# Performance work log

Measured on AMD Instinct MI355X. Metric: run time of the kernel, lower is better.

Reference implementation:

```python
import math
import jax, jax.numpy as jnp
import numpy as np

E = 24  # num experts


def layer_norm(x, w, b, eps=1e-6):
    m = x.mean(-1, keepdims=True)
    v = x.var(-1, keepdims=True)
    return (x - m) / jnp.sqrt(v + eps) * w + b


def top2_dispatch(x, Wg, C):
    # x: [S, d] -> combine/dispatch: [S, E, C] (GShard/DeepSpeed top-2 gating)
    logits = x @ Wg                                   # [S, E]
    gates = jax.nn.softmax(logits, axis=-1)
    idx1 = jnp.argmax(gates, axis=-1)
    m1 = jax.nn.one_hot(idx1, E, dtype=x.dtype)       # [S, E]
    masked = jnp.where(m1 > 0, -jnp.inf, logits)
    idx2 = jnp.argmax(masked, axis=-1)
    m2 = jax.nn.one_hot(idx2, E, dtype=x.dtype)
    # position of each token within its expert's capacity buffer
    loc1 = jnp.cumsum(m1, axis=0) - m1
    loc2 = jnp.cumsum(m2, axis=0) - m2 + jnp.sum(m1, axis=0, keepdims=True)
    m1 = m1 * (loc1 < C)                              # drop overflow tokens
    m2 = m2 * (loc2 < C)
    g1 = jnp.sum(gates * m1, axis=-1)
    g2 = jnp.sum(gates * m2, axis=-1)
    denom = jnp.maximum(g1 + g2, 1e-9)
    g1, g2 = g1 / denom, g2 / denom
    p1 = jnp.sum(loc1 * m1, axis=-1).astype(jnp.int32)
    p2 = jnp.sum(loc2 * m2, axis=-1).astype(jnp.int32)
    c1 = g1[:, None, None] * m1[:, :, None] * jax.nn.one_hot(p1, C, dtype=x.dtype)[:, None, :]
    c2 = g2[:, None, None] * m2[:, :, None] * jax.nn.one_hot(p2, C, dtype=x.dtype)[:, None, :]
    combine = c1 + c2                                  # [S, E, C]
    dispatch = (combine > 0).astype(x.dtype)
    return combine, dispatch


def moe_apply(x, combine, dispatch, W, b):
    # dispatch tokens to expert buffers, per-expert GEMM, combine back
    disp = jnp.einsum('sec,sd->ecd', dispatch, x)      # [E, C, d]
    h = jnp.einsum('ecd,edf->ecf', disp, W) + b[:, None, :]
    return jnp.einsum('sec,ecf->sf', combine, h)       # [S, f]


def setup_inputs() -> dict:
    b, seq, d_in, d_hid = 4, 2048, 1024, 4096
    ks = jax.random.split(jax.random.key(0), 6)
    s = 0.02
    return {
        'x': jax.random.normal(ks[0], (b, seq, d_in), dtype=jnp.float32),
        'Wg': jax.random.normal(ks[1], (d_in, E), dtype=jnp.float32) * s,
        'W1': jax.random.normal(ks[2], (E, d_in, d_hid), dtype=jnp.float32) * s,
        'b1': jnp.zeros((E, d_hid), dtype=jnp.float32),
        'W2': jax.random.normal(ks[3], (E, d_hid, d_in), dtype=jnp.float32) * s,
        'b2': jnp.zeros((E, d_in), dtype=jnp.float32),
        'ln_hid_w': jnp.ones((4, d_hid), dtype=jnp.float32),
        'ln_hid_b': jnp.zeros((4, d_hid), dtype=jnp.float32),
        'ln_out_w': jnp.ones((d_in,), dtype=jnp.float32),
        'ln_out_b': jnp.zeros((d_in,), dtype=jnp.float32),
    }


def reference(x, Wg, W1, b1, W2, b2, ln_hid_w, ln_hid_b, ln_out_w, ln_out_b):
    bsz, seq, d = x.shape
    H = 4
    n = seq // H
    S = bsz * n  # tokens per sub-sequence MoE call
    C = math.ceil(2 * S / E)  # top-2 capacity, capacity_factor=1.0
    # b (h n) c -> h (b n) c
    xg = x.reshape(bsz, H, n, d).transpose(1, 0, 2, 3).reshape(H, S, d)

    def per_group(xf, lw, lb):
        combine, dispatch = top2_dispatch(xf, Wg, C)
        h = moe_apply(xf, combine, dispatch, W1, b1)       # [S, d_hid]
        h = layer_norm(h, lw, lb)
        h = jax.nn.relu(h)                                  # dropout = identity (eval)
        return moe_apply(h, combine, dispatch, W2, b2)      # reuse gate_decision

    out = jax.vmap(per_group)(xg, ln_hid_w, ln_hid_b)       # [H, S, d]
    out = out.reshape(H, bsz, n, d).transpose(1, 0, 2, 3).reshape(bsz, seq, d)
    return layer_norm(out + x, ln_out_w, ln_out_b)
```

## Files before the change

### kernel.cpp

```cpp
#include <hip/hip_runtime.h>
#include <cstdint>
#include <cstddef>

#define E_      24
#define D_IN    1024
#define D_HID   4096
#define HGRP    4
#define BSZ     4
#define SEQ     2048
#define NSUB    512
#define S_      2048
#define NTOKG   8192
#define CAP     171
#define MR      768
#define MTILE   3
#define KSPL2   4

typedef __attribute__((ext_vector_type(4))) float          f32x4;
typedef __attribute__((ext_vector_type(4))) unsigned short u16x4;
typedef __attribute__((ext_vector_type(8))) unsigned short u16x8;
typedef __attribute__((ext_vector_type(4))) unsigned int   u32x4;
typedef __attribute__((ext_vector_type(8))) short          s16x8;

__device__ __forceinline__ unsigned short f2bf(float f) {
  unsigned int u = __float_as_uint(f);
  u += 0x7fffu + ((u >> 16) & 1u);
  return (unsigned short)(u >> 16);
}
__device__ __forceinline__ float bf2f(unsigned short v) {
  return __uint_as_float(((unsigned int)v) << 16);
}

__global__ __launch_bounds__(64)
void k_gating(const float* __restrict__ x, const float* __restrict__ Wg,
              int* __restrict__ tokE1, int* __restrict__ tokE2,
              float* __restrict__ tokG1, float* __restrict__ tokG2) {
  int tg = blockIdx.x;
  int h = tg >> 11, s = tg & 2047;
  int bi = s >> 9, ni = s & 511;
  const float* xr = x + ((size_t)bi*SEQ + (size_t)h*NSUB + ni) * D_IN;
  int lane = threadIdx.x;
  float acc[E_];
  #pragma unroll
  for (int e = 0; e < E_; ++e) acc[e] = 0.f;
  #pragma unroll
  for (int it = 0; it < D_IN/256; ++it) {
    f32x4 xv = *(const f32x4*)(xr + it*256 + lane*4);
    #pragma unroll
    for (int j = 0; j < 4; ++j) {
      float xs = xv[j];
      const float* wrow = Wg + (size_t)(it*256 + lane*4 + j) * E_;
      #pragma unroll
      for (int e = 0; e < E_; ++e) acc[e] += xs * wrow[e];
    }
  }
  #pragma unroll
  for (int e = 0; e < E_; ++e) {
    float v = acc[e];
    v += __shfl_xor(v, 32); v += __shfl_xor(v, 16); v += __shfl_xor(v, 8);
    v += __shfl_xor(v, 4);  v += __shfl_xor(v, 2);  v += __shfl_xor(v, 1);
    acc[e] = v;
  }
  if (lane == 0) {
    float mx = acc[0];
    #pragma unroll
    for (int e = 1; e < E_; ++e) mx = fmaxf(mx, acc[e]);
    float den = 0.f;
    #pragma unroll
    for (int e = 0; e < E_; ++e) den += expf(acc[e] - mx);
    int i1 = 0; float v1 = acc[0];
    #pragma unroll
    for (int e = 1; e < E_; ++e) if (acc[e] > v1) { v1 = acc[e]; i1 = e; }
    int i2 = -1; float v2 = -3.4e38f;
    #pragma unroll
    for (int e = 0; e < E_; ++e) if (e != i1 && acc[e] > v2) { v2 = acc[e]; i2 = e; }
    tokE1[tg] = i1; tokE2[tg] = i2;
    tokG1[tg] = expf(v1 - mx) / den;
    tokG2[tg] = expf(v2 - mx) / den;
  }
}

__global__ void k_init_slots(int* __restrict__ slotTok) {
  slotTok[blockIdx.x*256 + threadIdx.x] = -1;
}

__global__ __launch_bounds__(64)
void k_scan(const int* __restrict__ tokE1, const int* __restrict__ tokE2,
            float* __restrict__ tokG1, float* __restrict__ tokG2,
            int* __restrict__ tokP1, int* __restrict__ tokP2,
            int* __restrict__ slotTok) {
  int h = blockIdx.x;
  int lane = threadIdx.x;
  __shared__ int cnt[64][E_];
  __shared__ int tot1[E_];
  const int CH = S_/64;
  const int* e1 = tokE1 + h*S_;
  const int* e2 = tokE2 + h*S_;
  #pragma unroll
  for (int e = 0; e < E_; ++e) cnt[lane][e] = 0;
  __syncthreads();
  for (int k = 0; k < CH; ++k) cnt[lane][e1[lane*CH + k]]++;
  __syncthreads();
  if (lane < E_) {
    int run = 0;
    for (int j = 0; j < 64; ++j) { int t = cnt[j][lane]; cnt[j][lane] = run; run += t; }
    tot1[lane] = run;
  }
  __syncthreads();
  for (int k = 0; k < CH; ++k) {
    int s = lane*CH + k;
    int e = e1[s];
    int p = cnt[lane][e]++;
    int tg = h*S_ + s;
    if (p < CAP) { tokP1[tg] = p; slotTok[e*MR + h*CAP + p] = tg; }
    else         { tokP1[tg] = -1; }
  }
  __syncthreads();
  #pragma unroll
  for (int e = 0; e < E_; ++e) cnt[lane][e] = 0;
  __syncthreads();
  for (int k = 0; k < CH; ++k) cnt[lane][e2[lane*CH + k]]++;
  __syncthreads();
  if (lane < E_) {
    int run = tot1[lane];
    for (int j = 0; j < 64; ++j) { int t = cnt[j][lane]; cnt[j][lane] = run; run += t; }
  }
  __syncthreads();
  for (int k = 0; k < CH; ++k) {
    int s = lane*CH + k;
    int e = e2[s];
    int p = cnt[lane][e]++;
    int tg = h*S_ + s;
    if (p < CAP) { tokP2[tg] = p; slotTok[e*MR + h*CAP + p] = tg; }
    else         { tokP2[tg] = -1; }
  }
  __syncthreads();
  for (int k = 0; k < CH; ++k) {
    int tg = h*S_ + k*64 + lane;
    float g1 = (tokP1[tg] >= 0) ? tokG1[tg] : 0.f;
    float g2 = (tokP2[tg] >= 0) ? tokG2[tg] : 0.f;
    float den = fmaxf(g1 + g2, 1e-9f);
    tokG1[tg] = g1 / den;
    tokG2[tg] = g2 / den;
  }
}

__global__ __launch_bounds__(256)
void k_gather1(const float* __restrict__ x, const int* __restrict__ slotTok,
               unsigned short* __restrict__ A1) {
  int row = blockIdx.x;
  int tok = slotTok[row];
  int t = threadIdx.x;
  int k = t*4;
  int ba = ((k & 63)*2) ^ ((row & 7) << 4);
  char* dst = (char*)A1 + (size_t)row*(D_IN*2) + (size_t)(k >> 6)*128 + ba;
  u16x4 pk;
  if (tok >= 0) {
    int h = tok >> 11, s = tok & 2047;
    int bi = s >> 9, ni = s & 511;
    const float* xr = x + ((size_t)bi*SEQ + (size_t)h*NSUB + ni) * D_IN;
    f32x4 v = *(const f32x4*)(xr + k);
    pk.x = f2bf(v.x); pk.y = f2bf(v.y); pk.z = f2bf(v.z); pk.w = f2bf(v.w);
  } else {
    pk.x = 0; pk.y = 0; pk.z = 0; pk.w = 0;
  }
  *(u16x4*)dst = pk;
}

template<int K, int N>
__global__ __launch_bounds__(256)
void k_cvtW(const float* __restrict__ W, unsigned short* __restrict__ Wt) {
  const int NB = N/64, KB = K/64;
  int bid = blockIdx.x;
  int kb = bid % KB;
  int rem = bid / KB;
  int nb = rem % NB;
  int e  = rem / NB;
  __shared__ float lds[64][65];
  int t = threadIdx.x;
  int kl = t >> 2, ng = (t & 3) * 16;
  const float* src = W + ((size_t)e*K + (size_t)kb*64 + kl)*N + (size_t)nb*64 + ng;
  f32x4 v0 = *(const f32x4*)(src);
  f32x4 v1 = *(const f32x4*)(src + 4);
  f32x4 v2 = *(const f32x4*)(src + 8);
  f32x4 v3 = *(const f32x4*)(src + 12);
  #pragma unroll
  for (int j = 0; j < 4; ++j) lds[ng +  0 + j][kl] = v0[j];
  #pragma unroll
  for (int j = 0; j < 4; ++j) lds[ng +  4 + j][kl] = v1[j];
  #pragma unroll
  for (int j = 0; j < 4; ++j) lds[ng +  8 + j][kl] = v2[j];
  #pragma unroll
  for (int j = 0; j < 4; ++j) lds[ng + 12 + j][kl] = v3[j];
  __syncthreads();
  int nl = t >> 2, kg = (t & 3) * 16;
  u16x8 c0, c1;
  #pragma unroll
  for (int j = 0; j < 8; ++j) {
    c0[j] = f2bf(lds[nl][kg + j]);
    c1[j] = f2bf(lds[nl][kg + 8 + j]);
  }
  char* dst = (char*)Wt + ((size_t)e*N + (size_t)nb*64 + nl)*(K*2) + (size_t)kb*128;
  int sw = (nl & 7) << 4;
  *(u16x8*)(dst + ((kg*2)      ^ sw)) = c0;
  *(u16x8*)(dst + ((kg*2 + 16) ^ sw)) = c1;
}

template<int KROW, int KCHUNK, int N>
__global__ __launch_bounds__(512, 2)
void k_gemm(const unsigned short* __restrict__ A, const unsigned short* __restrict__ Wt,
            const float* __restrict__ bias, unsigned short* __restrict__ Out) {
  const int NT = N / 256;
  const int KSPLIT = KROW / KCHUNK;
  const int NKT = KCHUNK / 64;
  int cpx = gridDim.x >> 3;
  int lb = blockIdx.x;
  int bid = (lb & 7) * cpx + (lb >> 3);
  int mt  = bid % MTILE;
  int rem = bid / MTILE;
  int kc  = rem % KSPLIT;
  rem /= KSPLIT;
  int nt  = rem % NT;
  int e   = rem / NT;

  const char* Ab = (const char*)A  + ((size_t)e*MR + (size_t)mt*256) * (KROW*2);
  const char* Bb = (const char*)Wt + ((size_t)e*N  + (size_t)nt*256) * (KROW*2);
  size_t kbase = (size_t)kc * (KCHUNK*2);

  __shared__ unsigned short As0[256*64];
  __shared__ unsigned short As1[256*64];
  __shared__ unsigned short Bs0[256*64];
  __shared__ unsigned short Bs1[256*64];

  int tid  = threadIdx.x;
  int lane = tid & 63;
  int wid  = tid >> 6;
  int wr = wid >> 2, wc = wid & 3;

  f32x4 acc[8][4];
  #pragma unroll
  for (int i = 0; i < 8; ++i)
    #pragma unroll
    for (int j = 0; j < 4; ++j) acc[i][j] = (f32x4)0.f;

  auto stage = [&](int kt2, unsigned short* As, unsigned short* Bs) {
    size_t koff = kbase + (size_t)kt2*128;
    #pragma unroll
    for (int i = 0; i < 4; ++i) {
      int L = i*8192 + tid*16;
      __builtin_amdgcn_global_load_lds(
          (const __attribute__((address_space(1))) void*)(Ab + (size_t)(L >> 7)*(KROW*2) + koff + (L & 127)),
          (__attribute__((address_space(3))) void*)((char*)As + L), 16, 0, 0);
    }
    #pragma unroll
    for (int i = 0; i < 4; ++i) {
      int L = i*8192 + tid*16;
      __builtin_amdgcn_global_load_lds(
          (const __attribute__((address_space(1))) void*)(Bb + (size_t)(L >> 7)*(KROW*2) + koff + (L & 127)),
          (__attribute__((address_space(3))) void*)((char*)Bs + L), 16, 0, 0);
    }
  };
  auto fragsA = [&](const unsigned short* As, int ra, int ks, s16x8* afr) {
    int kb = ks*64 + (lane >> 4)*16;
    #pragma unroll
    for (int i = 0; i < 4; ++i) {
      int r = wr*128 + ra*64 + i*16 + (lane & 15);
      afr[i] = *(const s16x8*)((const char*)As + r*128 + (kb ^ ((r & 7) << 4)));
    }
  };
  auto fragsB = [&](const unsigned short* Bs, int ks, s16x8* bfr) {
    int kb = ks*64 + (lane >> 4)*16;
    #pragma unroll
    for (int j = 0; j < 4; ++j) {
      int c = wc*64 + j*16 + (lane & 15);
      bfr[j] = *(const s16x8*)((const char*)Bs + c*128 + (kb ^ ((c & 7) << 4)));
    }
  };
  auto mfma16 = [&](int ra, const s16x8* afr, const s16x8* bfr) {
    __builtin_amdgcn_s_setprio(1);
    #pragma unroll
    for (int i = 0; i < 4; ++i)
      #pragma unroll
      for (int j = 0; j < 4; ++j)
        acc[ra*4+i][j] = __builtin_amdgcn_mfma_f32_16x16x32_bf16(afr[i], bfr[j], acc[ra*4+i][j], 0, 0, 0);
    __builtin_amdgcn_s_setprio(0);
  };

  auto tile = [&](int t, const unsigned short* Ac, const unsigned short* Bc,
                  unsigned short* An, unsigned short* Bn) {
    int tn = (t + 1 < NKT) ? t + 1 : t;
    s16x8 afr[4], bfr[4];
    stage(tn, An, Bn);
    fragsA(Ac, 0, 0, afr); fragsB(Bc, 0, bfr);
    __builtin_amdgcn_s_barrier();
    asm volatile("s_waitcnt lgkmcnt(0)" ::: "memory");
    __builtin_amdgcn_sched_barrier(0);
    mfma16(0, afr, bfr);
    __builtin_amdgcn_s_barrier();
    fragsA(Ac, 1, 0, afr);
    __builtin_amdgcn_s_barrier();
    asm volatile("s_waitcnt lgkmcnt(0)" ::: "memory");
    __builtin_amdgcn_sched_barrier(0);
    mfma16(1, afr, bfr);
    __builtin_amdgcn_s_barrier();
    fragsA(Ac, 0, 1, afr); fragsB(Bc, 1, bfr);
    __builtin_amdgcn_s_barrier();
    asm volatile("s_waitcnt lgkmcnt(0)" ::: "memory");
    __builtin_amdgcn_sched_barrier(0);
    mfma16(0, afr, bfr);
    __builtin_amdgcn_s_barrier();
    fragsA(Ac, 1, 1, afr);
    __builtin_amdgcn_s_barrier();
    asm volatile("s_waitcnt lgkmcnt(0)" ::: "memory");
    __builtin_amdgcn_sched_barrier(0);
    mfma16(1, afr, bfr);
    __syncthreads();
  };

  stage(0, As0, Bs0);
  __syncthreads();
  for (int kt = 0; kt < NKT; kt += 2) {
    tile(kt,     As0, Bs0, As1, Bs1);
    tile(kt + 1, As1, Bs1, As0, Bs0);
  }

  unsigned short* Op = Out + (size_t)kc * ((size_t)E_*MR*N);
  #pragma unroll
  for (int j = 0; j < 4; ++j) {
    int col = nt*256 + wc*64 + j*16 + (lane & 15);
    float bv = (kc == 0) ? bias[(size_t)e*N + col] : 0.f;
    #pragma unroll
    for (int i = 0; i < 8; ++i) {
      int rowb = mt*256 + wr*128 + i*16 + (lane >> 4)*4;
      #pragma unroll
      for (int r = 0; r < 4; ++r) {
        float v = acc[i][j][r] + bv;
        Op[(size_t)e*MR*N + (size_t)(rowb + r)*N + col] = f2bf(v);
      }
    }
  }
}

__global__ __launch_bounds__(256)
void k_zero_empty(const int* __restrict__ slotTok, unsigned short* __restrict__ A2) {
  int row = blockIdx.x;
  if (slotTok[row] >= 0) return;
  u32x4 z = (u32x4)0u;
  char* base = (char*)A2 + (size_t)row*(D_HID*2) + threadIdx.x*32;
  *(u32x4*)base = z;
  *(u32x4*)(base + 16) = z;
}

__global__ __launch_bounds__(256)
void k_combine_ln(const unsigned short* __restrict__ H1,
                  const int* __restrict__ tokE1, const int* __restrict__ tokE2,
                  const int* __restrict__ tokP1, const int* __restrict__ tokP2,
                  const float* __restrict__ tokG1, const float* __restrict__ tokG2,
                  const float* __restrict__ lnw, const float* __restrict__ lnb,
                  unsigned short* __restrict__ A2) {
  int tg = blockIdx.x;
  int h = tg >> 11;
  int p1 = tokP1[tg], p2 = tokP2[tg];
  if (p1 < 0 && p2 < 0) return;
  float g1 = tokG1[tg], g2 = tokG2[tg];
  long r1 = (p1 >= 0) ? ((long)tokE1[tg]*MR + h*CAP + p1) : -1;
  long r2 = (p2 >= 0) ? ((long)tokE2[tg]*MR + h*CAP + p2) : -1;
  int t = threadIdx.x;
  float v[16];
  float sum = 0.f, sq = 0.f;
  #pragma unroll
  for (int u = 0; u < 4; ++u) {
    int f = u*1024 + t*4;
    float a0 = 0.f, a1 = 0.f, a2 = 0.f, a3 = 0.f;
    if (r1 >= 0) {
      u16x4 q = *(const u16x4*)(H1 + (size_t)r1*D_HID + f);
      a0 += g1*bf2f(q.x); a1 += g1*bf2f(q.y); a2 += g1*bf2f(q.z); a3 += g1*bf2f(q.w);
    }
    if (r2 >= 0) {
      u16x4 q = *(const u16x4*)(H1 + (size_t)r2*D_HID + f);
      a0 += g2*bf2f(q.x); a1 += g2*bf2f(q.y); a2 += g2*bf2f(q.z); a3 += g2*bf2f(q.w);
    }
    v[u*4+0] = a0; v[u*4+1] = a1; v[u*4+2] = a2; v[u*4+3] = a3;
    sum += a0 + a1 + a2 + a3;
    sq  += a0*a0 + a1*a1 + a2*a2 + a3*a3;
  }
  #pragma unroll
  for (int o = 32; o; o >>= 1) { sum += __shfl_xor(sum, o); sq += __shfl_xor(sq, o); }
  __shared__ float redA[4], redB[4];
  int wid = t >> 6;
  if ((t & 63) == 0) { redA[wid] = sum; redB[wid] = sq; }
  __syncthreads();
  float S = redA[0] + redA[1] + redA[2] + redA[3];
  float Q = redB[0] + redB[1] + redB[2] + redB[3];
  float m = S * (1.f / D_HID);
  float var = Q * (1.f / D_HID) - m*m;
  float rs = rsqrtf(var + 1e-6f);
  #pragma unroll
  for (int u = 0; u < 4; ++u) {
    int f = u*1024 + t*4;
    u16x4 pk;
    float y0 = fmaxf((v[u*4+0]-m)*rs*lnw[h*D_HID+f+0] + lnb[h*D_HID+f+0], 0.f);
    float y1 = fmaxf((v[u*4+1]-m)*rs*lnw[h*D_HID+f+1] + lnb[h*D_HID+f+1], 0.f);
    float y2 = fmaxf((v[u*4+2]-m)*rs*lnw[h*D_HID+f+2] + lnb[h*D_HID+f+2], 0.f);
    float y3 = fmaxf((v[u*4+3]-m)*rs*lnw[h*D_HID+f+3] + lnb[h*D_HID+f+3], 0.f);
    pk.x = f2bf(y0); pk.y = f2bf(y1); pk.z = f2bf(y2); pk.w = f2bf(y3);
    int chunk = f >> 6;
    int ob = (f & 63)*2;
    if (r1 >= 0)
      *(u16x4*)((char*)A2 + (size_t)r1*(D_HID*2) + (size_t)chunk*128 + (ob ^ (((int)r1 & 7) << 4))) = pk;
    if (r2 >= 0)
      *(u16x4*)((char*)A2 + (size_t)r2*(D_HID*2) + (size_t)chunk*128 + (ob ^ (((int)r2 & 7) << 4))) = pk;
  }
}

__global__ __launch_bounds__(256)
void k_final(const unsigned short* __restrict__ H2p, const float* __restrict__ x,
             const int* __restrict__ tokE1, const int* __restrict__ tokE2,
             const int* __restrict__ tokP1, const int* __restrict__ tokP2,
             const float* __restrict__ tokG1, const float* __restrict__ tokG2,
             const float* __restrict__ lnw, const float* __restrict__ lnb,
             float* __restrict__ out) {
  const size_t PSTR = (size_t)E_*MR*D_IN;
  int tg = blockIdx.x;
  int h = tg >> 11, s = tg & 2047;
  int bi = s >> 9, ni = s & 511;
  size_t xoff = ((size_t)bi*SEQ + (size_t)h*NSUB + ni) * D_IN;
  int p1 = tokP1[tg], p2 = tokP2[tg];
  float g1 = tokG1[tg], g2 = tokG2[tg];
  int t = threadIdx.x;
  int f = t*4;
  f32x4 xv = *(const f32x4*)(x + xoff + f);
  float v0 = xv.x, v1 = xv.y, v2 = xv.z, v3 = xv.w;
  if (p1 >= 0) {
    size_t r1 = (size_t)tokE1[tg]*MR + h*CAP + p1;
    float a0 = 0.f, a1 = 0.f, a2 = 0.f, a3 = 0.f;
    #pragma unroll
    for (int p = 0; p < KSPL2; ++p) {
      u16x4 q = *(const u16x4*)(H2p + p*PSTR + r1*D_IN + f);
      a0 += bf2f(q.x); a1 += bf2f(q.y); a2 += bf2f(q.z); a3 += bf2f(q.w);
    }
    v0 += g1*a0; v1 += g1*a1; v2 += g1*a2; v3 += g1*a3;
  }
  if (p2 >= 0) {
    size_t r2 = (size_t)tokE2[tg]*MR + h*CAP + p2;
    float a0 = 0.f, a1 = 0.f, a2 = 0.f, a3 = 0.f;
    #pragma unroll
    for (int p = 0; p < KSPL2; ++p) {
      u16x4 q = *(const u16x4*)(H2p + p*PSTR + r2*D_IN + f);
      a0 += bf2f(q.x); a1 += bf2f(q.y); a2 += bf2f(q.z); a3 += bf2f(q.w);
    }
    v0 += g2*a0; v1 += g2*a1; v2 += g2*a2; v3 += g2*a3;
  }
  float sum = v0+v1+v2+v3, sq = v0*v0+v1*v1+v2*v2+v3*v3;
  #pragma unroll
  for (int o = 32; o; o >>= 1) { sum += __shfl_xor(sum, o); sq += __shfl_xor(sq, o); }
  __shared__ float redA[4], redB[4];
  int wid = t >> 6;
  if ((t & 63) == 0) { redA[wid] = sum; redB[wid] = sq; }
  __syncthreads();
  float S = redA[0] + redA[1] + redA[2] + redA[3];
  float Q = redB[0] + redB[1] + redB[2] + redB[3];
  float m = S * (1.f / D_IN);
  float var = Q * (1.f / D_IN) - m*m;
  float rs = rsqrtf(var + 1e-6f);
  f32x4 res;
  res.x = (v0 - m)*rs*lnw[f+0] + lnb[f+0];
  res.y = (v1 - m)*rs*lnw[f+1] + lnb[f+1];
  res.z = (v2 - m)*rs*lnw[f+2] + lnb[f+2];
  res.w = (v3 - m)*rs*lnw[f+3] + lnb[f+3];
  *(f32x4*)(out + xoff + f) = res;
}

extern "C" void kernel_launch(void* const* d_in, const int* in_sizes, int n_in,
                              void* d_out, int out_size, void* d_ws, size_t ws_size,
                              hipStream_t stream) {
  const float* x    = (const float*)d_in[0];
  const float* Wg   = (const float*)d_in[1];
  const float* W1   = (const float*)d_in[2];
  const float* b1   = (const float*)d_in[3];
  const float* W2   = (const float*)d_in[4];
  const float* b2   = (const float*)d_in[5];
  const float* lnhw = (const float*)d_in[6];
  const float* lnhb = (const float*)d_in[7];
  const float* lnow = (const float*)d_in[8];
  const float* lnob = (const float*)d_in[9];
  float* out = (float*)d_out;
  (void)in_sizes; (void)n_in; (void)out_size; (void)ws_size;

  char* ws = (char*)d_ws;
  size_t off = 0;
  auto take = [&](size_t bytes) -> char* {
    char* p = ws + off;
    off += (bytes + 255) & ~(size_t)255;
    return p;
  };
  int*   tokE1 = (int*)take(NTOKG*sizeof(int));
  int*   tokE2 = (int*)take(NTOKG*sizeof(int));
  int*   tokP1 = (int*)take(NTOKG*sizeof(int));
  int*   tokP2 = (int*)take(NTOKG*sizeof(int));
  float* tokG1 = (float*)take(NTOKG*sizeof(float));
  float* tokG2 = (float*)take(NTOKG*sizeof(float));
  int*   slotTok = (int*)take((size_t)E_*MR*sizeof(int));
  unsigned short* A1 = (unsigned short*)take((size_t)E_*MR*D_IN*2);
  unsigned short* H1 = (unsigned short*)take((size_t)E_*MR*D_HID*2);
  unsigned short* A2 = (unsigned short*)take((size_t)E_*MR*D_HID*2);
  unsigned short* Wt = (unsigned short*)take((size_t)E_*D_IN*D_HID*2);
  unsigned short* H2p = H1;

  k_init_slots<<<dim3(E_*MR/256), dim3(256), 0, stream>>>(slotTok);
  k_gating<<<dim3(NTOKG), dim3(64), 0, stream>>>(x, Wg, tokE1, tokE2, tokG1, tokG2);
  k_scan<<<dim3(HGRP), dim3(64), 0, stream>>>(tokE1, tokE2, tokG1, tokG2, tokP1, tokP2, slotTok);
  k_gather1<<<dim3(E_*MR), dim3(256), 0, stream>>>(x, slotTok, A1);
  k_cvtW<D_IN, D_HID><<<dim3(E_*(D_HID/64)*(D_IN/64)), dim3(256), 0, stream>>>(W1, Wt);
  k_gemm<D_IN, D_IN, D_HID><<<dim3(E_*(D_HID/256)*MTILE), dim3(512), 0, stream>>>(A1, Wt, b1, H1);
  k_zero_empty<<<dim3(E_*MR), dim3(256), 0, stream>>>(slotTok, A2);
  k_combine_ln<<<dim3(NTOKG), dim3(256), 0, stream>>>(H1, tokE1, tokE2, tokP1, tokP2,
                                                      tokG1, tokG2, lnhw, lnhb, A2);
  k_cvtW<D_HID, D_IN><<<dim3(E_*(D_IN/64)*(D_HID/64)), dim3(256), 0, stream>>>(W2, Wt);
  k_gemm<D_HID, D_IN, D_IN><<<dim3(E_*(D_IN/256)*MTILE*KSPL2), dim3(512), 0, stream>>>(A2, Wt, b2, H2p);
  k_final<<<dim3(NTOKG), dim3(256), 0, stream>>>(H2p, x, tokE1, tokE2, tokP1, tokP2,
                                                 tokG1, tokG2, lnow, lnob, out);
}
```

Baseline: 898.1 us.

## Interleave GEMM global-to-LDS staging with MFMA phases and use partial vmcnt waits

The GEMM main loop no longer issues all eight global-to-LDS loads for the next tile at once and ends each tile with a full __syncthreads. The loads are split into per-slice calls spread across the four MFMA phases, with `s_waitcnt vmcnt(2)` plus barriers so only the slices needed next must be resident. This lets A rows 64-127 and 192-255 stay in flight across the tile boundary. Separately, the weight-conversion kernel now reads rows with 16 threads per row in float4 chunks, giving more contiguous global loads. The risk is subtle ordering bugs, because vmcnt counts only the issuing wave's own loads and the scheme relies on the slice-to-row mapping.

```diff
diff --git a/kernel.cpp b/kernel.cpp
--- a/kernel.cpp
+++ b/kernel.cpp
@@ -178,20 +178,15 @@
   int e  = rem / NB;
   __shared__ float lds[64][65];
   int t = threadIdx.x;
-  int kl = t >> 2, ng = (t & 3) * 16;
-  const float* src = W + ((size_t)e*K + (size_t)kb*64 + kl)*N + (size_t)nb*64 + ng;
-  f32x4 v0 = *(const f32x4*)(src);
-  f32x4 v1 = *(const f32x4*)(src + 4);
-  f32x4 v2 = *(const f32x4*)(src + 8);
-  f32x4 v3 = *(const f32x4*)(src + 12);
-  #pragma unroll
-  for (int j = 0; j < 4; ++j) lds[ng +  0 + j][kl] = v0[j];
-  #pragma unroll
-  for (int j = 0; j < 4; ++j) lds[ng +  4 + j][kl] = v1[j];
-  #pragma unroll
-  for (int j = 0; j < 4; ++j) lds[ng +  8 + j][kl] = v2[j];
-  #pragma unroll
-  for (int j = 0; j < 4; ++j) lds[ng + 12 + j][kl] = v3[j];
+  int rl = t >> 4;
+  int cl = (t & 15) * 4;
+  const float* base = W + ((size_t)e*K + (size_t)kb*64)*N + (size_t)nb*64;
+  #pragma unroll
+  for (int p = 0; p < 4; ++p) {
+    int r = p*16 + rl;
+    f32x4 v = *(const f32x4*)(base + (size_t)r*N + cl);
+    lds[cl+0][r] = v.x; lds[cl+1][r] = v.y; lds[cl+2][r] = v.z; lds[cl+3][r] = v.w;
+  }
   __syncthreads();
   int nl = t >> 2, kg = (t & 3) * 16;
   u16x8 c0, c1;
@@ -243,22 +238,19 @@
     #pragma unroll
     for (int j = 0; j < 4; ++j) acc[i][j] = (f32x4)0.f;
 
-  auto stage = [&](int kt2, unsigned short* As, unsigned short* Bs) {
+  auto stageAi = [&](int kt2, unsigned short* As, int i) {
     size_t koff = kbase + (size_t)kt2*128;
-    #pragma unroll
-    for (int i = 0; i < 4; ++i) {
-      int L = i*8192 + tid*16;
-      __builtin_amdgcn_global_load_lds(
-          (const __attribute__((address_space(1))) void*)(Ab + (size_t)(L >> 7)*(KROW*2) + koff + (L & 127)),
-          (__attribute__((address_space(3))) void*)((char*)As + L), 16, 0, 0);
-    }
-    #pragma unroll
-    for (int i = 0; i < 4; ++i) {
-      int L = i*8192 + tid*16;
-      __builtin_amdgcn_global_load_lds(
-          (const __attribute__((address_space(1))) void*)(Bb + (size_t)(L >> 7)*(KROW*2) + koff + (L & 127)),
-          (__attribute__((address_space(3))) void*)((char*)Bs + L), 16, 0, 0);
-    }
+    int L = i*8192 + tid*16;
+    __builtin_amdgcn_global_load_lds(
+        (const __attribute__((address_space(1))) void*)(Ab + (size_t)(L >> 7)*(KROW*2) + koff + (L & 127)),
+        (__attribute__((address_space(3))) void*)((char*)As + L), 16, 0, 0);
+  };
+  auto stageBi = [&](int kt2, unsigned short* Bs, int i) {
+    size_t koff = kbase + (size_t)kt2*128;
+    int L = i*8192 + tid*16;
+    __builtin_amdgcn_global_load_lds(
+        (const __attribute__((address_space(1))) void*)(Bb + (size_t)(L >> 7)*(KROW*2) + koff + (L & 127)),
+        (__attribute__((address_space(3))) void*)((char*)Bs + L), 16, 0, 0);
   };
   auto fragsA = [&](const unsigned short* As, int ra, int ks, s16x8* afr) {
     int kb = ks*64 + (lane >> 4)*16;
@@ -286,42 +278,52 @@
     __builtin_amdgcn_s_setprio(0);
   };
 
-  auto tile = [&](int t, const unsigned short* Ac, const unsigned short* Bc,
-                  unsigned short* An, unsigned short* Bn) {
-    int tn = (t + 1 < NKT) ? t + 1 : t;
+  unsigned short *Acur = As0, *Anxt = As1, *Bcur = Bs0, *Bnxt = Bs1;
+
+  stageBi(0, Bcur, 0); stageBi(0, Bcur, 1); stageBi(0, Bcur, 2); stageBi(0, Bcur, 3);
+  stageAi(0, Acur, 0); stageAi(0, Acur, 2);
+  stageAi(0, Acur, 1); stageAi(0, Acur, 3);
+  asm volatile("s_waitcnt vmcnt(2)" ::: "memory");
+  __builtin_amdgcn_sched_barrier(0);
+  __builtin_amdgcn_s_barrier();
+
+  for (int kt = 0; kt < NKT; ++kt) {
+    int tn = (kt + 1 < NKT) ? kt + 1 : kt;
     s16x8 afr[4], bfr[4];
-    stage(tn, An, Bn);
-    fragsA(Ac, 0, 0, afr); fragsB(Bc, 0, bfr);
+    fragsA(Acur, 0, 0, afr); fragsB(Bcur, 0, bfr);
+    stageBi(tn, Bnxt, 0); stageBi(tn, Bnxt, 1);
+    asm volatile("s_waitcnt vmcnt(2)" ::: "memory");
+    __builtin_amdgcn_sched_barrier(0);
     __builtin_amdgcn_s_barrier();
     asm volatile("s_waitcnt lgkmcnt(0)" ::: "memory");
     __builtin_amdgcn_sched_barrier(0);
     mfma16(0, afr, bfr);
     __builtin_amdgcn_s_barrier();
-    fragsA(Ac, 1, 0, afr);
+    fragsA(Acur, 1, 0, afr);
+    stageBi(tn, Bnxt, 2); stageBi(tn, Bnxt, 3);
     __builtin_amdgcn_s_barrier();
     asm volatile("s_waitcnt lgkmcnt(0)" ::: "memory");
     __builtin_amdgcn_sched_barrier(0);
     mfma16(1, afr, bfr);
     __builtin_amdgcn_s_barrier();
-    fragsA(Ac, 0, 1, afr); fragsB(Bc, 1, bfr);
+    fragsA(Acur, 0, 1, afr); fragsB(Bcur, 1, bfr);
+    stageAi(tn, Anxt, 0); stageAi(tn, Anxt, 2);
     __builtin_amdgcn_s_barrier();
     asm volatile("s_waitcnt lgkmcnt(0)" ::: "memory");
     __builtin_amdgcn_sched_barrier(0);
     mfma16(0, afr, bfr);
     __builtin_amdgcn_s_barrier();
-    fragsA(Ac, 1, 1, afr);
+    fragsA(Acur, 1, 1, afr);
+    stageAi(tn, Anxt, 1); stageAi(tn, Anxt, 3);
     __builtin_amdgcn_s_barrier();
     asm volatile("s_waitcnt lgkmcnt(0)" ::: "memory");
     __builtin_amdgcn_sched_barrier(0);
     mfma16(1, afr, bfr);
-    __syncthreads();
-  };
-
-  stage(0, As0, Bs0);
-  __syncthreads();
-  for (int kt = 0; kt < NKT; kt += 2) {
-    tile(kt,     As0, Bs0, As1, Bs1);
-    tile(kt + 1, As1, Bs1, As0, Bs0);
+    asm volatile("s_waitcnt vmcnt(2)" ::: "memory");
+    __builtin_amdgcn_sched_barrier(0);
+    __builtin_amdgcn_s_barrier();
+    unsigned short* t1 = Acur; Acur = Anxt; Anxt = t1;
+    unsigned short* t2 = Bcur; Bcur = Bnxt; Bnxt = t2;
   }
 
   unsigned short* Op = Out + (size_t)kc * ((size_t)E_*MR*N);
```

Result: faster. 875.5 us (-2.5%).
